# Performance work log

Hardware: AMD Instinct MI355X
Metric: run time of the kernel (lower is better)

## Reference

```python
import jax, jax.numpy as jnp
import numpy as np

C_Z = 128
C_HIDDEN = 32
N_HEAD = 4
HC = N_HEAD * C_HIDDEN  # 128
LN_EPS = 1e-5


def setup_inputs() -> dict:
    key = jax.random.key(0)
    ks = jax.random.split(key, 8)
    b, n = 1, 256
    s = 1.0 / np.sqrt(C_Z)
    return {
        "z_ij": jax.random.normal(ks[0], (b, n, n, C_Z), dtype=jnp.float32),
        "ln_gamma": jnp.ones((C_Z,), dtype=jnp.float32),
        "ln_beta": jnp.zeros((C_Z,), dtype=jnp.float32),
        "Wq": jax.random.normal(ks[1], (C_Z, HC), dtype=jnp.float32) * s,
        "Wk": jax.random.normal(ks[2], (C_Z, HC), dtype=jnp.float32) * s,
        "Wv": jax.random.normal(ks[3], (C_Z, HC), dtype=jnp.float32) * s,
        "Wb": jax.random.normal(ks[4], (C_Z, N_HEAD), dtype=jnp.float32) * s,
        "Wg": jax.random.normal(ks[5], (C_Z, HC), dtype=jnp.float32) * s,
        "Wout": jax.random.normal(ks[6], (HC, C_Z), dtype=jnp.float32) * (1.0 / np.sqrt(HC)),
    }


def reference(z_ij, ln_gamma, ln_beta, Wq, Wk, Wv, Wb, Wg, Wout):
    b, n, _, _ = z_ij.shape
    # LayerNorm over c_z
    mu = jnp.mean(z_ij, axis=-1, keepdims=True)
    var = jnp.var(z_ij, axis=-1, keepdims=True)
    z = (z_ij - mu) * jax.lax.rsqrt(var + LN_EPS) * ln_gamma + ln_beta

    def heads(x):  # [b,i,j,hc] -> [b,i,j,h,d]
        return x.reshape(b, n, n, N_HEAD, C_HIDDEN)

    q = heads(z @ Wq)
    k = heads(z @ Wk)
    v = heads(z @ Wv)
    bias = z @ Wb                      # [b,i,j,h]
    g = jax.nn.sigmoid(heads(z @ Wg))  # [b,i,j,h,d]

    scores = jnp.einsum('bijhd,bikhd->bijkh', q, k) / np.sqrt(C_HIDDEN)
    scores = scores + bias[:, None]    # bias[b, j, k, h] broadcast over i
    a = jax.nn.softmax(scores, axis=-2)  # over k
    o = jnp.einsum('bijkh,bikhd->bijhd', a, v)
    o = (g * o).reshape(b, n, n, HC)
    return o @ Wout
```

## Files before the change

kernel.cpp:

```cpp
#include <hip/hip_runtime.h>

typedef _Float16 f16x8 __attribute__((ext_vector_type(8)));
typedef _Float16 f16x4 __attribute__((ext_vector_type(4)));
typedef float f32x4 __attribute__((ext_vector_type(4)));

#define MFMA16(a, b, c) __builtin_amdgcn_mfma_f32_16x16x32_f16(a, b, c, 0, 0, 0)
#define SEGB 16777216ull

#define QSCALE ((float)(1.4426950408889634 * 0.17677669529663687))
#define LOG2E 1.4426950408889634f

__global__ __launch_bounds__(256) void k_ln(
    const float* __restrict__ z, const float* __restrict__ gamma,
    const float* __restrict__ beta,
    const float* __restrict__ Wq, const float* __restrict__ Wk,
    const float* __restrict__ Wv, const float* __restrict__ Wg,
    const float* __restrict__ Wout, const float* __restrict__ Wb,
    _Float16* __restrict__ zln, _Float16* __restrict__ WtAll)
{
  __shared__ _Float16 sw[32 * 136];
  int bid = blockIdx.x;
  if (bid < 8192) {
    int lane = threadIdx.x & 63;
    int w = threadIdx.x >> 6;
    int half = lane >> 5, lh = lane & 31;
    int row = bid * 8 + w * 2 + half;
    float4 v = ((const float4*)(z + (size_t)row * 128))[lh];
    float s = v.x + v.y + v.z + v.w;
    #pragma unroll
    for (int m = 1; m < 32; m <<= 1) s += __shfl_xor(s, m);
    float mu = s * 0.0078125f;
    float d0 = v.x - mu, d1 = v.y - mu, d2 = v.z - mu, d3 = v.w - mu;
    float q = d0 * d0 + d1 * d1 + d2 * d2 + d3 * d3;
    #pragma unroll
    for (int m = 1; m < 32; m <<= 1) q += __shfl_xor(q, m);
    float rs = rsqrtf(q * 0.0078125f + 1e-5f);
    float4 g4 = ((const float4*)gamma)[lh];
    float4 b4 = ((const float4*)beta)[lh];
    f16x4 o;
    o[0] = (_Float16)(d0 * rs * g4.x + b4.x);
    o[1] = (_Float16)(d1 * rs * g4.y + b4.y);
    o[2] = (_Float16)(d2 * rs * g4.z + b4.z);
    o[3] = (_Float16)(d3 * rs * g4.w + b4.w);
    *(f16x4*)(zln + (size_t)row * 128 + lh * 4) = o;
  } else if (bid < 8212) {
    int t = bid - 8192;
    int mat = t >> 2, n0 = (t & 3) * 32;
    const float* src = (mat == 0) ? Wq : (mat == 1) ? Wk : (mat == 2) ? Wv
                       : (mat == 3) ? Wg : Wout;
    float sc = (mat == 0) ? QSCALE : 1.0f;
    for (int it = 0; it < 16; ++it) {
      int e = threadIdx.x + it * 256;
      int c = e >> 5, j = e & 31;
      sw[j * 136 + c] = (_Float16)(src[c * 128 + n0 + j] * sc);
    }
    __syncthreads();
    for (int it = 0; it < 2; ++it) {
      int ch = threadIdx.x + it * 256;
      int n = ch >> 4, k8 = (ch & 15) * 8;
      *(int4*)(WtAll + mat * 16384 + (n0 + n) * 128 + k8) =
          *(const int4*)&sw[n * 136 + k8];
    }
  } else {
    _Float16* WbT = WtAll + 5 * 16384;
    for (int it = 0; it < 8; ++it) {
      int e = threadIdx.x + it * 256;
      if (e < 2048) {
        int hrow = e >> 7, k = e & 127;
        float v = (hrow < 4) ? Wb[k * 4 + hrow] * LOG2E : 0.0f;
        WbT[hrow * 128 + k] = (_Float16)v;
      }
    }
  }
}

__global__ __launch_bounds__(256, 3) void k_proj(
    const _Float16* __restrict__ A, const _Float16* __restrict__ WtAll,
    _Float16* __restrict__ Qb, _Float16* __restrict__ Kb,
    _Float16* __restrict__ Vb, _Float16* __restrict__ Gb,
    _Float16* __restrict__ biasP)
{
  __shared__ _Float16 sA[128 * 136];
  int m0 = blockIdx.x * 128;
  int tid = threadIdx.x, lane = tid & 63, w = tid >> 6;
  int lr = lane & 15, lg = lane >> 4;
  for (int it = 0; it < 8; ++it) {
    int ch = tid + it * 256;
    int r = ch >> 4, c8 = (ch & 15) * 8;
    *(int4*)&sA[r * 136 + c8] = *(const int4*)(A + (size_t)(m0 + r) * 128 + c8);
  }
  __syncthreads();
  f32x4 z4 = {0.f, 0.f, 0.f, 0.f};
  #pragma unroll 1
  for (int mat = 0; mat < 4; ++mat) {
    const _Float16* Bt = WtAll + mat * 16384;
    _Float16* outp = (mat == 0) ? Qb : (mat == 1) ? Kb : (mat == 2) ? Vb : Gb;
    f32x4 acc[2][8];
    #pragma unroll
    for (int g = 0; g < 2; ++g)
      #pragma unroll
      for (int nt = 0; nt < 8; ++nt) acc[g][nt] = z4;
    #pragma unroll
    for (int k0 = 0; k0 < 128; k0 += 32) {
      f16x8 af[2], bf[8];
      #pragma unroll
      for (int g = 0; g < 2; ++g)
        af[g] = *(const f16x8*)&sA[(w * 32 + g * 16 + lr) * 136 + k0 + lg * 8];
      #pragma unroll
      for (int nt = 0; nt < 8; ++nt)
        bf[nt] = *(const f16x8*)(Bt + (nt * 16 + lr) * 128 + k0 + lg * 8);
      #pragma unroll
      for (int g = 0; g < 2; ++g)
        #pragma unroll
        for (int nt = 0; nt < 8; ++nt)
          acc[g][nt] = MFMA16(af[g], bf[nt], acc[g][nt]);
    }
    bool sig = (mat == 3);
    #pragma unroll
    for (int g = 0; g < 2; ++g)
      #pragma unroll
      for (int nt = 0; nt < 8; ++nt)
        #pragma unroll
        for (int r = 0; r < 4; ++r) {
          int row = m0 + w * 32 + g * 16 + lg * 4 + r;
          int col = nt * 16 + lr;
          float v = acc[g][nt][r];
          if (sig) v = 1.0f / (1.0f + __expf(-v));
          outp[(size_t)row * 128 + col] = (_Float16)v;
        }
  }
  {
    const _Float16* WbT = WtAll + 5 * 16384;
    f32x4 acc[2] = {z4, z4};
    #pragma unroll
    for (int k0 = 0; k0 < 128; k0 += 32) {
      f16x8 bfb = *(const f16x8*)(WbT + lr * 128 + k0 + lg * 8);
      #pragma unroll
      for (int g = 0; g < 2; ++g) {
        f16x8 afb = *(const f16x8*)&sA[(w * 32 + g * 16 + lr) * 136 + k0 + lg * 8];
        acc[g] = MFMA16(afb, bfb, acc[g]);
      }
    }
    if (lr < 4) {
      #pragma unroll
      for (int g = 0; g < 2; ++g)
        #pragma unroll
        for (int r = 0; r < 4; ++r) {
          int R = m0 + w * 32 + g * 16 + lg * 4 + r;
          biasP[lr * 65536 + (R >> 8) * 256 + (R & 15) * 16 + ((R >> 4) & 15)] =
              (_Float16)acc[g][r];
        }
    }
  }
}

__global__ __launch_bounds__(256, 3) void k_attn(
    const _Float16* __restrict__ Qb, const _Float16* __restrict__ Kb,
    const _Float16* __restrict__ Vb, const _Float16* __restrict__ biasP,
    _Float16* __restrict__ O)
{
  __shared__ _Float16 sK[256 * 32];
  __shared__ _Float16 sV[32 * 256];
  __shared__ _Float16 sP[64 * 256];
  int i = blockIdx.x, h = blockIdx.y;
  int tid = threadIdx.x;
  size_t base = ((size_t)i * 256) * 128 + h * 32;
  for (int it = 0; it < 4; ++it) {
    int ch = tid + it * 256;
    int r = ch >> 2, cx = ch & 3;
    int p = cx ^ ((r >> 1) & 3);
    *(int4*)&sK[r * 32 + p * 8] = *(const int4*)(Kb + base + (size_t)r * 128 + cx * 8);
  }
  for (int it = 0; it < 4; ++it) {
    int ch = tid + it * 256;
    int k = ch >> 2, d8 = (ch & 3) * 8;
    f16x8 tv = *(const f16x8*)(Vb + base + (size_t)k * 128 + d8);
    #pragma unroll
    for (int jj = 0; jj < 8; ++jj) {
      int d = d8 + jj;
      int p = (k >> 3) ^ (d & 7);
      sV[d * 256 + p * 8 + (k & 7)] = tv[jj];
    }
  }
  __syncthreads();
  int lane = tid & 63, w = tid >> 6;
  int lr = lane & 15, lg = lane >> 4;
  f32x4 z4 = {0.f, 0.f, 0.f, 0.f};
  const _Float16* bp = biasP + ((size_t)h << 16);
  for (int pass = 0; pass < 4; ++pass) {
    int jbase = pass * 64;
    int jq = jbase + w * 16 + lr;
    f16x8 aq = *(const f16x8*)(Qb + base + (size_t)jq * 128 + lg * 8);
    f16x8 bb0[4], bb1[4];
    #pragma unroll
    for (int r = 0; r < 4; ++r) {
      int j = jbase + w * 16 + lg * 4 + r;
      bb0[r] = *(const f16x8*)(bp + j * 256 + lr * 16);
      bb1[r] = *(const f16x8*)(bp + j * 256 + lr * 16 + 8);
    }
    float sum[4] = {0.f, 0.f, 0.f, 0.f};
    #pragma unroll
    for (int kt = 0; kt < 16; ++kt) {
      int kr = kt * 16 + lr;
      int p = lg ^ ((kr >> 1) & 3);
      f16x8 bk = *(const f16x8*)&sK[kr * 32 + p * 8];
      f32x4 s = MFMA16(aq, bk, z4);
      #pragma unroll
      for (int r = 0; r < 4; ++r) {
        float bb = (kt < 8) ? (float)bb0[r][kt & 7] : (float)bb1[r][kt & 7];
        float sv = fminf(s[r] + bb, 14.f);
        float e = exp2f(sv);
        sum[r] += e;
        int row = w * 16 + lg * 4 + r;
        int pch = ((kr >> 3) ^ (row & 7));
        sP[row * 256 + pch * 8 + (kr & 7)] = (_Float16)e;
      }
    }
    float rinv[4];
    #pragma unroll
    for (int r = 0; r < 4; ++r) {
      float sm = sum[r];
      #pragma unroll
      for (int m = 1; m < 16; m <<= 1) sm += __shfl_xor(sm, m);
      rinv[r] = 1.0f / sm;
    }
    f32x4 oacc[2] = {z4, z4};
    int prow = w * 16 + lr;
    #pragma unroll
    for (int ks = 0; ks < 8; ++ks) {
      int c = ks * 4 + lg;
      f16x8 ap = *(const f16x8*)&sP[prow * 256 + (c ^ (prow & 7)) * 8];
      #pragma unroll
      for (int nt = 0; nt < 2; ++nt) {
        int d = nt * 16 + lr;
        f16x8 bv = *(const f16x8*)&sV[d * 256 + (c ^ (d & 7)) * 8];
        oacc[nt] = MFMA16(ap, bv, oacc[nt]);
      }
    }
    #pragma unroll
    for (int nt = 0; nt < 2; ++nt)
      #pragma unroll
      for (int r = 0; r < 4; ++r) {
        int j = jbase + w * 16 + lg * 4 + r;
        int d = nt * 16 + lr;
        O[base + (size_t)j * 128 + d] = (_Float16)(oacc[nt][r] * rinv[r]);
      }
  }
}

__global__ __launch_bounds__(256, 3) void k_outp(
    const _Float16* __restrict__ O, const _Float16* __restrict__ G,
    const _Float16* __restrict__ Bt, float* __restrict__ out)
{
  int m0 = blockIdx.x * 64;
  int tid = threadIdx.x, lane = tid & 63, w = tid >> 6;
  int lr = lane & 15, lg = lane >> 4;
  f32x4 z4 = {0.f, 0.f, 0.f, 0.f};
  f32x4 acc[8];
  #pragma unroll
  for (int nt = 0; nt < 8; ++nt) acc[nt] = z4;
  #pragma unroll
  for (int k0 = 0; k0 < 128; k0 += 32) {
    size_t a = (size_t)(m0 + w * 16 + lr) * 128 + k0 + lg * 8;
    f16x8 o8 = *(const f16x8*)(O + a);
    f16x8 g8 = *(const f16x8*)(G + a);
    f16x8 af = o8 * g8;
    f16x8 bf[8];
    #pragma unroll
    for (int nt = 0; nt < 8; ++nt)
      bf[nt] = *(const f16x8*)(Bt + (nt * 16 + lr) * 128 + k0 + lg * 8);
    #pragma unroll
    for (int nt = 0; nt < 8; ++nt)
      acc[nt] = MFMA16(af, bf[nt], acc[nt]);
  }
  #pragma unroll
  for (int nt = 0; nt < 8; ++nt)
    #pragma unroll
    for (int r = 0; r < 4; ++r) {
      int row = m0 + w * 16 + lg * 4 + r;
      int col = nt * 16 + lr;
      out[(size_t)row * 128 + col] = acc[nt][r];
    }
}

extern "C" void kernel_launch(void* const* d_in, const int* in_sizes, int n_in,
                              void* d_out, int out_size, void* d_ws, size_t ws_size,
                              hipStream_t stream) {
  (void)in_sizes; (void)n_in; (void)out_size; (void)ws_size;
  const float* z    = (const float*)d_in[0];
  const float* gam  = (const float*)d_in[1];
  const float* bet  = (const float*)d_in[2];
  const float* Wq   = (const float*)d_in[3];
  const float* Wk   = (const float*)d_in[4];
  const float* Wv   = (const float*)d_in[5];
  const float* Wb   = (const float*)d_in[6];
  const float* Wg   = (const float*)d_in[7];
  const float* Wout = (const float*)d_in[8];

  char* ws = (char*)d_ws;
  _Float16* zln   = (_Float16*)(ws);
  _Float16* Qb    = (_Float16*)(ws + SEGB);
  _Float16* Kb    = (_Float16*)(ws + SEGB * 2);
  _Float16* Vb    = (_Float16*)(ws + SEGB * 3);
  _Float16* Gb    = (_Float16*)(ws + SEGB * 4);
  _Float16* biasP = (_Float16*)(ws + SEGB * 5);
  _Float16* WtAll = (_Float16*)(ws + SEGB * 5 + 1048576);

  k_ln<<<8213, 256, 0, stream>>>(z, gam, bet, Wq, Wk, Wv, Wg, Wout, Wb,
                                 zln, WtAll);
  k_proj<<<512, 256, 0, stream>>>(zln, WtAll, Qb, Kb, Vb, Gb, biasP);
  k_attn<<<dim3(256, 4), 256, 0, stream>>>(Qb, Kb, Vb, biasP, zln);
  k_outp<<<1024, 256, 0, stream>>>(zln, Gb, WtAll + 4 * 16384, (float*)d_out);
}
```

Baseline: 214.8 us.

## Swap MFMA operand order for row-contiguous vectorized stores and simpler bias layout

The MFMA A/B operands are swapped in the projection, attention and output kernels, so each lane holds four consecutive columns of one row. This turns strided scalar half and float stores into f16x4/float4 stores. The bias projection is now written in plain row-major [h][j*256+k] order, which lets attention read bias with one f16x4 load per tile and cuts the softmax row-sum shuffles to two. The projection tile shrinks to 64 rows across twice as many blocks, and launch bounds are retuned (proj/outp 4, attn 2). The attn change lets it use more registers per thread at the cost of fewer resident waves.

```diff
diff --git a/kernel.cpp b/kernel.cpp
--- a/kernel.cpp
+++ b/kernel.cpp
@@ -74,87 +74,73 @@
   }
 }
 
-__global__ __launch_bounds__(256, 3) void k_proj(
+__global__ __launch_bounds__(256, 4) void k_proj(
     const _Float16* __restrict__ A, const _Float16* __restrict__ WtAll,
     _Float16* __restrict__ Qb, _Float16* __restrict__ Kb,
     _Float16* __restrict__ Vb, _Float16* __restrict__ Gb,
     _Float16* __restrict__ biasP)
 {
-  __shared__ _Float16 sA[128 * 136];
-  int m0 = blockIdx.x * 128;
+  __shared__ _Float16 sA[64 * 136];
+  int m0 = blockIdx.x * 64;
   int tid = threadIdx.x, lane = tid & 63, w = tid >> 6;
   int lr = lane & 15, lg = lane >> 4;
-  for (int it = 0; it < 8; ++it) {
+  for (int it = 0; it < 4; ++it) {
     int ch = tid + it * 256;
     int r = ch >> 4, c8 = (ch & 15) * 8;
     *(int4*)&sA[r * 136 + c8] = *(const int4*)(A + (size_t)(m0 + r) * 128 + c8);
   }
   __syncthreads();
   f32x4 z4 = {0.f, 0.f, 0.f, 0.f};
+  int myrow = m0 + w * 16 + lr;
   #pragma unroll 1
   for (int mat = 0; mat < 4; ++mat) {
     const _Float16* Bt = WtAll + mat * 16384;
     _Float16* outp = (mat == 0) ? Qb : (mat == 1) ? Kb : (mat == 2) ? Vb : Gb;
-    f32x4 acc[2][8];
-    #pragma unroll
-    for (int g = 0; g < 2; ++g)
-      #pragma unroll
-      for (int nt = 0; nt < 8; ++nt) acc[g][nt] = z4;
+    f32x4 acc[8];
+    #pragma unroll
+    for (int nt = 0; nt < 8; ++nt) acc[nt] = z4;
     #pragma unroll
     for (int k0 = 0; k0 < 128; k0 += 32) {
-      f16x8 af[2], bf[8];
-      #pragma unroll
-      for (int g = 0; g < 2; ++g)
-        af[g] = *(const f16x8*)&sA[(w * 32 + g * 16 + lr) * 136 + k0 + lg * 8];
+      f16x8 af = *(const f16x8*)&sA[(w * 16 + lr) * 136 + k0 + lg * 8];
+      f16x8 bf[8];
       #pragma unroll
       for (int nt = 0; nt < 8; ++nt)
         bf[nt] = *(const f16x8*)(Bt + (nt * 16 + lr) * 128 + k0 + lg * 8);
       #pragma unroll
-      for (int g = 0; g < 2; ++g)
-        #pragma unroll
-        for (int nt = 0; nt < 8; ++nt)
-          acc[g][nt] = MFMA16(af[g], bf[nt], acc[g][nt]);
+      for (int nt = 0; nt < 8; ++nt)
+        acc[nt] = MFMA16(bf[nt], af, acc[nt]);
     }
     bool sig = (mat == 3);
     #pragma unroll
-    for (int g = 0; g < 2; ++g)
-      #pragma unroll
-      for (int nt = 0; nt < 8; ++nt)
-        #pragma unroll
-        for (int r = 0; r < 4; ++r) {
-          int row = m0 + w * 32 + g * 16 + lg * 4 + r;
-          int col = nt * 16 + lr;
-          float v = acc[g][nt][r];
-          if (sig) v = 1.0f / (1.0f + __expf(-v));
-          outp[(size_t)row * 128 + col] = (_Float16)v;
-        }
+    for (int nt = 0; nt < 8; ++nt) {
+      f16x4 o4;
+      #pragma unroll
+      for (int r = 0; r < 4; ++r) {
+        float v = acc[nt][r];
+        if (sig) v = 1.0f / (1.0f + __expf(-v));
+        o4[r] = (_Float16)v;
+      }
+      *(f16x4*)(outp + (size_t)myrow * 128 + nt * 16 + lg * 4) = o4;
+    }
   }
   {
     const _Float16* WbT = WtAll + 5 * 16384;
-    f32x4 acc[2] = {z4, z4};
+    f32x4 accb = z4;
     #pragma unroll
     for (int k0 = 0; k0 < 128; k0 += 32) {
       f16x8 bfb = *(const f16x8*)(WbT + lr * 128 + k0 + lg * 8);
-      #pragma unroll
-      for (int g = 0; g < 2; ++g) {
-        f16x8 afb = *(const f16x8*)&sA[(w * 32 + g * 16 + lr) * 136 + k0 + lg * 8];
-        acc[g] = MFMA16(afb, bfb, acc[g]);
-      }
-    }
-    if (lr < 4) {
-      #pragma unroll
-      for (int g = 0; g < 2; ++g)
-        #pragma unroll
-        for (int r = 0; r < 4; ++r) {
-          int R = m0 + w * 32 + g * 16 + lg * 4 + r;
-          biasP[lr * 65536 + (R >> 8) * 256 + (R & 15) * 16 + ((R >> 4) & 15)] =
-              (_Float16)acc[g][r];
-        }
-    }
-  }
-}
-
-__global__ __launch_bounds__(256, 3) void k_attn(
+      f16x8 afb = *(const f16x8*)&sA[(w * 16 + lr) * 136 + k0 + lg * 8];
+      accb = MFMA16(bfb, afb, accb);
+    }
+    if (lg == 0) {
+      #pragma unroll
+      for (int r = 0; r < 4; ++r)
+        biasP[r * 65536 + myrow] = (_Float16)accb[r];
+    }
+  }
+}
+
+__global__ __launch_bounds__(256, 2) void k_attn(
     const _Float16* __restrict__ Qb, const _Float16* __restrict__ Kb,
     const _Float16* __restrict__ Vb, const _Float16* __restrict__ biasP,
     _Float16* __restrict__ O)
@@ -189,79 +175,69 @@
   const _Float16* bp = biasP + ((size_t)h << 16);
   for (int pass = 0; pass < 4; ++pass) {
     int jbase = pass * 64;
-    int jq = jbase + w * 16 + lr;
-    f16x8 aq = *(const f16x8*)(Qb + base + (size_t)jq * 128 + lg * 8);
-    f16x8 bb0[4], bb1[4];
-    #pragma unroll
-    for (int r = 0; r < 4; ++r) {
-      int j = jbase + w * 16 + lg * 4 + r;
-      bb0[r] = *(const f16x8*)(bp + j * 256 + lr * 16);
-      bb1[r] = *(const f16x8*)(bp + j * 256 + lr * 16 + 8);
-    }
-    float sum[4] = {0.f, 0.f, 0.f, 0.f};
+    int j = jbase + w * 16 + lr;
+    int row = w * 16 + lr;
+    f16x8 aq = *(const f16x8*)(Qb + base + (size_t)j * 128 + lg * 8);
+    const _Float16* brow = bp + j * 256;
+    float sum = 0.f;
     #pragma unroll
     for (int kt = 0; kt < 16; ++kt) {
       int kr = kt * 16 + lr;
       int p = lg ^ ((kr >> 1) & 3);
       f16x8 bk = *(const f16x8*)&sK[kr * 32 + p * 8];
-      f32x4 s = MFMA16(aq, bk, z4);
+      f32x4 s = MFMA16(bk, aq, z4);
+      f16x4 bb = *(const f16x4*)(brow + kt * 16 + lg * 4);
+      f16x4 pk;
       #pragma unroll
       for (int r = 0; r < 4; ++r) {
-        float bb = (kt < 8) ? (float)bb0[r][kt & 7] : (float)bb1[r][kt & 7];
-        float sv = fminf(s[r] + bb, 14.f);
+        float sv = fminf(s[r] + (float)bb[r], 14.f);
         float e = exp2f(sv);
-        sum[r] += e;
-        int row = w * 16 + lg * 4 + r;
-        int pch = ((kr >> 3) ^ (row & 7));
-        sP[row * 256 + pch * 8 + (kr & 7)] = (_Float16)e;
-      }
-    }
-    float rinv[4];
-    #pragma unroll
-    for (int r = 0; r < 4; ++r) {
-      float sm = sum[r];
-      #pragma unroll
-      for (int m = 1; m < 16; m <<= 1) sm += __shfl_xor(sm, m);
-      rinv[r] = 1.0f / sm;
-    }
+        sum += e;
+        pk[r] = (_Float16)e;
+      }
+      int ch = kt * 2 + (lg >> 1);
+      *(f16x4*)&sP[row * 256 + (ch ^ (row & 7)) * 8 + (lg & 1) * 4] = pk;
+    }
+    sum += __shfl_xor(sum, 16);
+    sum += __shfl_xor(sum, 32);
+    float rinv = 1.0f / sum;
     f32x4 oacc[2] = {z4, z4};
-    int prow = w * 16 + lr;
     #pragma unroll
     for (int ks = 0; ks < 8; ++ks) {
       int c = ks * 4 + lg;
-      f16x8 ap = *(const f16x8*)&sP[prow * 256 + (c ^ (prow & 7)) * 8];
+      f16x8 ap = *(const f16x8*)&sP[row * 256 + (c ^ (row & 7)) * 8];
       #pragma unroll
       for (int nt = 0; nt < 2; ++nt) {
         int d = nt * 16 + lr;
         f16x8 bv = *(const f16x8*)&sV[d * 256 + (c ^ (d & 7)) * 8];
-        oacc[nt] = MFMA16(ap, bv, oacc[nt]);
-      }
-    }
-    #pragma unroll
-    for (int nt = 0; nt < 2; ++nt)
-      #pragma unroll
-      for (int r = 0; r < 4; ++r) {
-        int j = jbase + w * 16 + lg * 4 + r;
-        int d = nt * 16 + lr;
-        O[base + (size_t)j * 128 + d] = (_Float16)(oacc[nt][r] * rinv[r]);
-      }
-  }
-}
-
-__global__ __launch_bounds__(256, 3) void k_outp(
+        oacc[nt] = MFMA16(bv, ap, oacc[nt]);
+      }
+    }
+    #pragma unroll
+    for (int nt = 0; nt < 2; ++nt) {
+      f16x4 o4;
+      #pragma unroll
+      for (int r = 0; r < 4; ++r) o4[r] = (_Float16)(oacc[nt][r] * rinv);
+      *(f16x4*)(O + base + (size_t)j * 128 + nt * 16 + lg * 4) = o4;
+    }
+  }
+}
+
+__global__ __launch_bounds__(256, 4) void k_outp(
     const _Float16* __restrict__ O, const _Float16* __restrict__ G,
     const _Float16* __restrict__ Bt, float* __restrict__ out)
 {
   int m0 = blockIdx.x * 64;
   int tid = threadIdx.x, lane = tid & 63, w = tid >> 6;
   int lr = lane & 15, lg = lane >> 4;
+  int myrow = m0 + w * 16 + lr;
   f32x4 z4 = {0.f, 0.f, 0.f, 0.f};
   f32x4 acc[8];
   #pragma unroll
   for (int nt = 0; nt < 8; ++nt) acc[nt] = z4;
   #pragma unroll
   for (int k0 = 0; k0 < 128; k0 += 32) {
-    size_t a = (size_t)(m0 + w * 16 + lr) * 128 + k0 + lg * 8;
+    size_t a = (size_t)myrow * 128 + k0 + lg * 8;
     f16x8 o8 = *(const f16x8*)(O + a);
     f16x8 g8 = *(const f16x8*)(G + a);
     f16x8 af = o8 * g8;
@@ -271,16 +247,15 @@
       bf[nt] = *(const f16x8*)(Bt + (nt * 16 + lr) * 128 + k0 + lg * 8);
     #pragma unroll
     for (int nt = 0; nt < 8; ++nt)
-      acc[nt] = MFMA16(af, bf[nt], acc[nt]);
+      acc[nt] = MFMA16(bf[nt], af, acc[nt]);
   }
   #pragma unroll
-  for (int nt = 0; nt < 8; ++nt)
-    #pragma unroll
-    for (int r = 0; r < 4; ++r) {
-      int row = m0 + w * 16 + lg * 4 + r;
-      int col = nt * 16 + lr;
-      out[(size_t)row * 128 + col] = acc[nt][r];
-    }
+  for (int nt = 0; nt < 8; ++nt) {
+    float4 o4;
+    o4.x = acc[nt][0]; o4.y = acc[nt][1];
+    o4.z = acc[nt][2]; o4.w = acc[nt][3];
+    *(float4*)(out + (size_t)myrow * 128 + nt * 16 + lg * 4) = o4;
+  }
 }
 
 extern "C" void kernel_launch(void* const* d_in, const int* in_sizes, int n_in,
@@ -308,7 +283,7 @@
 
   k_ln<<<8213, 256, 0, stream>>>(z, gam, bet, Wq, Wk, Wv, Wg, Wout, Wb,
                                  zln, WtAll);
-  k_proj<<<512, 256, 0, stream>>>(zln, WtAll, Qb, Kb, Vb, Gb, biasP);
+  k_proj<<<1024, 256, 0, stream>>>(zln, WtAll, Qb, Kb, Vb, Gb, biasP);
   k_attn<<<dim3(256, 4), 256, 0, stream>>>(Qb, Kb, Vb, biasP, zln);
   k_outp<<<1024, 256, 0, stream>>>(zln, Gb, WtAll + 4 * 16384, (float*)d_out);
 }
```

Result: slower. 241.2 us (+12.3%).
